# Performance work log

Measured on AMD Instinct MI355X. Metric: run time of the kernel, lower is better.

Reference implementation:

```python
import jax, jax.numpy as jnp
import numpy as np
from jax import lax

H = 1024
D = 128
T = 64  # n_step + n_middle


def gru_cell(x, h, w_ih, w_hh, b_ih, b_hh):
    # torch.nn.GRUCell gate order: r, z, n
    gi = x @ w_ih.T + b_ih
    gh = h @ w_hh.T + b_hh
    ir, iz, i_n = jnp.split(gi, 3, axis=-1)
    hr, hz, h_n = jnp.split(gh, 3, axis=-1)
    r = jax.nn.sigmoid(ir + hr)
    z = jax.nn.sigmoid(iz + hz)
    n = jnp.tanh(i_n + r * h_n)
    return (1.0 - z) * n + z * h


def decoder(z_seq, z8, n1, w_init, b_init, wi1, wh1, bi1, bh1, wi2, wh2, bi2, bh2, w_out, b_out):
    B = z_seq.shape[0]
    out0 = jnp.zeros((B, D), z_seq.dtype).at[:, -1].set(1.0)
    h0 = z8 @ w_init.T + b_init              # [B, H]
    h1 = jnp.zeros_like(h0)                  # replaced at i == 0
    xs = (jnp.arange(T), jnp.swapaxes(z_seq, 0, 1))  # ([T], [T, B, D])

    def step(carry, x):
        h0, h1, out = carry
        i, z_i = x
        inp = jnp.where(i <= n1 - 1, z_i, out)
        h0n = gru_cell(inp, h0, wi1, wh1, bi1, bh1)
        h1 = jnp.where(i == 0, h0n, h1)
        h1n = gru_cell(h0n, h1, wi2, wh2, bi2, bh2)
        out = h1n @ w_out.T + b_out          # [B, 128]
        return (h0n, h1n, out), out

    _, outs = lax.scan(step, (h0, h1, out0), xs)  # [T, B, 128]
    return jnp.swapaxes(outs[n1 - 1:], 0, 1)      # [B, T-n1+1, 128]


def _p(key, shape):
    return jax.random.normal(key, shape, dtype=jnp.float32) * 0.02


def setup_inputs() -> dict:
    key = jax.random.key(0)
    ks = jax.random.split(key, 32)
    B = 2048
    inp = {
        'zp': jax.random.normal(ks[0], (B, T, D), jnp.float32),
        'zr': jax.random.normal(ks[1], (B, T, D), jnp.float32),
        'zp8': jax.random.normal(ks[2], (B, D), jnp.float32),
        'zr8': jax.random.normal(ks[3], (B, D), jnp.float32),
        'n1': 16,
        'n2': 48,
    }
    # GRU cells 1..4: (w_ih [3H, in], w_hh [3H, H], b_ih [3H], b_hh [3H])
    for j, name in enumerate(['1', '2', '3', '4']):
        in_dim = D if name in ('1', '3') else H
        inp['wi' + name] = _p(ks[4 + 4 * j], (3 * H, in_dim))
        inp['wh' + name] = _p(ks[5 + 4 * j], (3 * H, H))
        inp['bi' + name] = _p(ks[6 + 4 * j], (3 * H,))
        inp['bh' + name] = _p(ks[7 + 4 * j], (3 * H,))
    inp['w_init0'] = _p(ks[20], (H, D)); inp['b_init0'] = _p(ks[21], (H,))
    inp['w_init1'] = _p(ks[22], (H, D)); inp['b_init1'] = _p(ks[23], (H,))
    inp['w_out0'] = _p(ks[24], (D, H)); inp['b_out0'] = _p(ks[25], (D,))
    inp['w_out1'] = _p(ks[26], (D, H)); inp['b_out1'] = _p(ks[27], (D,))
    return inp


def reference(zp, zr, zp8, zr8, n1, n2,
              wi1, wh1, bi1, bh1, wi2, wh2, bi2, bh2,
              wi3, wh3, bi3, bh3, wi4, wh4, bi4, bh4,
              w_init0, b_init0, w_init1, b_init1,
              w_out0, b_out0, w_out1, b_out1):
    z_r = decoder(zr, zr8, n1, w_init0, b_init0, wi1, wh1, bi1, bh1,
                  wi2, wh2, bi2, bh2, w_out0, b_out0)
    z_p = decoder(zp, zp8, n1, w_init1, b_init1, wi3, wh3, bi3, bh3,
                  wi4, wh4, bi4, bh4, w_out1, b_out1)
    return (z_p, z_r)
```

## Files before the change

kernel.cpp:

```cpp
#include <hip/hip_runtime.h>

typedef unsigned short u16;
typedef unsigned int u32;
typedef __attribute__((ext_vector_type(8))) short short8;
typedef __attribute__((ext_vector_type(4))) float f32x4;

#define DEV __device__ __forceinline__
#define SB0() __builtin_amdgcn_sched_barrier(0)

DEV u16 f2bf(float f){
  u32 u = __builtin_bit_cast(u32, f);
  u += 0x7fffu + ((u >> 16) & 1u);
  return (u16)(u >> 16);
}
DEV float sigm(float x){ return 1.f / (1.f + __expf(-x)); }
DEV float tanh_(float x){ return 2.f / (1.f + __expf(-2.f * x)) - 1.f; }

DEV void gl_lds16(const void* g, void* l){
  __builtin_amdgcn_global_load_lds(
      (const __attribute__((address_space(1))) u32*)g,
      (__attribute__((address_space(3))) u32*)l, 16, 0, 0);
}

#define MFMA16(A,B,C) __builtin_amdgcn_mfma_f32_16x16x32_bf16(A, B, C, 0, 0, 0)

__global__ void pack_w_kernel(const float* __restrict__ wi, const float* __restrict__ wh,
                              u16* __restrict__ dst, int Ki, int Kh, int nrows){
  const int KT = Ki + Kh;
  const long n = (long)nrows * KT;
  for (long idx = (long)blockIdx.x * blockDim.x + threadIdx.x; idx < n;
       idx += (long)gridDim.x * blockDim.x){
    int r = (int)(idx / KT), c = (int)(idx % KT);
    float v = (c < Ki) ? wi[(long)r * Ki + c] : wh[(long)r * Kh + (c - Ki)];
    dst[idx] = f2bf(v);
  }
}

struct InitA { const float* z8; const float* wini; const float* bini; float* h0f; u16* h0bf; };

__global__ __launch_bounds__(256)
void init_kernel(InitA A0, InitA A1){
  const InitA& a = (blockIdx.z == 0) ? A0 : A1;
  __shared__ float lz[64][128];
  const int tid = threadIdx.x;
  const int rb = blockIdx.x * 64, ub = blockIdx.y * 128;
  {
    const int row = tid >> 2, q = tid & 3;
    const float4* p = (const float4*)(a.z8 + (long)(rb + row) * 128 + q * 32);
    float4* dst = (float4*)&lz[row][q * 32];
    #pragma unroll
    for (int j = 0; j < 8; ++j) dst[j] = p[j];
  }
  __syncthreads();
  const int u = ub + (tid & 127);
  const int rg = tid >> 7;
  float acc[32];
  #pragma unroll
  for (int r = 0; r < 32; ++r) acc[r] = 0.f;
  for (int k = 0; k < 128; k += 4){
    float4 w4 = *(const float4*)&a.wini[(long)u * 128 + k];
    #pragma unroll
    for (int r = 0; r < 32; ++r){
      float4 z4 = *(const float4*)&lz[rg * 32 + r][k];
      acc[r] += w4.x * z4.x + w4.y * z4.y + w4.z * z4.z + w4.w * z4.w;
    }
  }
  const float b = a.bini[u];
  #pragma unroll
  for (int r = 0; r < 32; ++r){
    const long row = rb + rg * 32 + r;
    const float v = acc[r] + b;
    a.h0f[row * 1024 + u] = v;
    a.h0bf[row * 1024 + u] = f2bf(v);
  }
}

struct CellA {
  const u16* W;
  const float* bi; const float* bh;
  const float* afz; const float* afo;
  const u16* ab1; const u16* ab2;
  const float* holdr; float* holdw; u16* hbfw;
};

template<int CELL>
__global__ __attribute__((amdgpu_waves_per_eu(2, 2))) __launch_bounds__(256)
void cell_kernel(CellA A0, CellA A1, const int* dn1, int step){
  constexpr int KTOT = (CELL == 1) ? 1152 : 2048;
  constexpr int KT = KTOT / 64;
  constexpr int NI_STEPS = (CELL == 1) ? 2 : 16;

  __shared__ u16 lA[2][128 * 64];
  __shared__ u16 lB[2][192 * 64];

  const CellA& a = (blockIdx.y == 0) ? A0 : A1;
  const int tid = threadIdx.x;
  const int lane = tid & 63;
  const int wv = tid >> 6;
  const int wm = wv >> 1;
  const int wn = wv & 1;
  const int bid = blockIdx.x;
  const int inner = bid >> 3;
  const int m_idx = inner & 15;
  const int n_idx = (bid & 7) * 2 + (inner >> 4);
  const int brow = m_idx * 128;
  const int u0 = n_idx * 64;

  f32x4 aR[4][2] = {}; f32x4 aZ[4][2] = {};
  f32x4 aNI[4][2] = {}; f32x4 aNH[4][2] = {};

  const int srow = tid >> 3;
  const int sxor8 = ((tid & 7) ^ (srow & 7)) * 8;

  auto stage = [&](int bf, int kt){
    const int k0 = kt * 64;
    const u16* ab; int kk;
    if constexpr (CELL == 1){ ab = a.ab1; kk = k0 - 128; }
    else { if (k0 < 1024){ ab = a.ab1; kk = k0; } else { ab = a.ab2; kk = k0 - 1024; } }
    #pragma unroll
    for (int j = 0; j < 4; ++j)
      gl_lds16(ab + (long)(brow + j * 32 + srow) * 1024 + kk + sxor8,
               &lA[bf][(j * 32 + wv * 8) * 64]);
    #pragma unroll
    for (int j = 0; j < 6; ++j){
      const int gbase = j * 32 + wv * 8;
      const int g = gbase >> 6;
      gl_lds16(a.W + (long)(g * 1024 + u0 + ((j * 32 + srow) & 63)) * KTOT + k0 + sxor8,
               &lB[bf][(j * 32 + wv * 8) * 64]);
    }
  };

  const int l15 = lane & 15;
  const int kq = lane >> 4;
  const int sx = lane & 7;

  auto read_a_ks = [&](int bf, int ks, short8 (&af)[4]){
    const int soff = (((ks * 4 + kq) ^ sx)) * 8;
    #pragma unroll
    for (int fr = 0; fr < 4; ++fr)
      af[fr] = *(const short8*)&lA[bf][(wm * 64 + fr * 16 + l15) * 64 + soff];
  };
  auto read_b_ks = [&](int bf, int g, int ks, short8 (&bg)[2]){
    const int soff = (((ks * 4 + kq) ^ sx)) * 8;
    #pragma unroll
    for (int fc = 0; fc < 2; ++fc)
      bg[fc] = *(const short8*)&lB[bf][(g * 64 + wn * 32 + fc * 16 + l15) * 64 + soff];
  };
  auto mfma8 = [&](const short8 (&af)[4], const short8 (&bg)[2], f32x4 (&A)[4][2]){
    #pragma unroll
    for (int fr = 0; fr < 4; ++fr)
      #pragma unroll
      for (int fc = 0; fc < 2; ++fc)
        A[fr][fc] = MFMA16(af[fr], bg[fc], A[fr][fc]);
  };

  int kstart;
  if constexpr (CELL == 1){
    const int n1v = *dn1;
    const float* fsrc; long fstr;
    if (step < n1v){ fsrc = a.afz; fstr = 64 * 128; }
    else           { fsrc = a.afo; fstr = 128; }
    {
      const int row = tid >> 1, half = tid & 1;
      #pragma unroll
      for (int st = 0; st < 2; ++st){
        const float* pp = fsrc + (long)(brow + row) * fstr + st * 64 + half * 32;
        #pragma unroll
        for (int q = 0; q < 4; ++q){
          float4 x = ((const float4*)pp)[2 * q];
          float4 y = ((const float4*)pp)[2 * q + 1];
          short8 o;
          o[0] = (short)f2bf(x.x); o[1] = (short)f2bf(x.y);
          o[2] = (short)f2bf(x.z); o[3] = (short)f2bf(x.w);
          o[4] = (short)f2bf(y.x); o[5] = (short)f2bf(y.y);
          o[6] = (short)f2bf(y.z); o[7] = (short)f2bf(y.w);
          const int s = half * 4 + q;
          *(short8*)&lA[st][row * 64 + ((s ^ (row & 7)) * 8)] = o;
        }
        #pragma unroll
        for (int j = 0; j < 6; ++j){
          const int gbase = j * 32 + wv * 8;
          const int g = gbase >> 6;
          gl_lds16(a.W + (long)(g * 1024 + u0 + ((j * 32 + srow) & 63)) * KTOT + st * 64 + sxor8,
                   &lB[st][(j * 32 + wv * 8) * 64]);
        }
      }
    }
    __syncthreads();
    #pragma unroll
    for (int st = 0; st < 2; ++st){
      short8 af0[4], af1[4], b0[2], b1[2];
      read_a_ks(st, 0, af0); read_a_ks(st, 1, af1);
      read_b_ks(st, 0, 0, b0); read_b_ks(st, 0, 1, b1);
      asm volatile("s_waitcnt lgkmcnt(0)" ::: "memory"); SB0();
      mfma8(af0, b0, aR); mfma8(af1, b1, aR);
      read_b_ks(st, 1, 0, b0); read_b_ks(st, 1, 1, b1);
      asm volatile("s_waitcnt lgkmcnt(0)" ::: "memory"); SB0();
      mfma8(af0, b0, aZ); mfma8(af1, b1, aZ);
      read_b_ks(st, 2, 0, b0); read_b_ks(st, 2, 1, b1);
      asm volatile("s_waitcnt lgkmcnt(0)" ::: "memory"); SB0();
      mfma8(af0, b0, aNI); mfma8(af1, b1, aNI);
    }
    __syncthreads();
    stage(0, 2); stage(1, 3);
    kstart = 2;
  } else {
    stage(0, 0); stage(1, 1);
    kstart = 0;
  }

  for (int kt = kstart; kt < KT; ++kt){
    const int b = kt & 1;
    if (kt < KT - 1) asm volatile("s_waitcnt vmcnt(10)" ::: "memory");
    else             asm volatile("s_waitcnt vmcnt(0)" ::: "memory");
    SB0();
    __builtin_amdgcn_s_barrier();
    SB0();
    short8 af0[4], af1[4], bR0[2], bR1[2], bZ0[2], bZ1[2], bN0[2], bN1[2];
    read_a_ks(b, 0, af0); read_b_ks(b, 0, 0, bR0); SB0();
    read_b_ks(b, 1, 0, bZ0); read_b_ks(b, 2, 0, bN0); SB0();
    read_a_ks(b, 1, af1); read_b_ks(b, 0, 1, bR1); SB0();
    asm volatile("s_waitcnt lgkmcnt(10)" ::: "memory"); SB0();
    __builtin_amdgcn_s_setprio(1);
    mfma8(af0, bR0, aR);
    __builtin_amdgcn_s_setprio(0); SB0();
    read_b_ks(b, 1, 1, bZ1); read_b_ks(b, 2, 1, bN1); SB0();
    asm volatile("s_waitcnt lgkmcnt(10)" ::: "memory"); SB0();
    __builtin_amdgcn_s_setprio(1);
    mfma8(af0, bZ0, aZ);
    if (kt < NI_STEPS) mfma8(af0, bN0, aNI); else mfma8(af0, bN0, aNH);
    __builtin_amdgcn_s_setprio(0); SB0();
    asm volatile("s_waitcnt lgkmcnt(4)" ::: "memory"); SB0();
    __builtin_amdgcn_s_setprio(1);
    mfma8(af1, bR1, aR);
    __builtin_amdgcn_s_setprio(0); SB0();
    asm volatile("s_waitcnt lgkmcnt(0)" ::: "memory"); SB0();
    __builtin_amdgcn_s_barrier();
    SB0();
    if (kt + 2 < KT) stage(b, kt + 2);
    __builtin_amdgcn_s_setprio(1);
    mfma8(af1, bZ1, aZ);
    if (kt < NI_STEPS) mfma8(af1, bN1, aNI); else mfma8(af1, bN1, aNH);
    __builtin_amdgcn_s_setprio(0);
  }

  const int rq = (lane >> 4) * 4;
  #pragma unroll
  for (int fc = 0; fc < 2; ++fc){
    const int u = u0 + wn * 32 + fc * 16 + l15;
    const float br = a.bi[u] + a.bh[u];
    const float bz = a.bi[1024 + u] + a.bh[1024 + u];
    const float bni = a.bi[2048 + u];
    const float bnh = a.bh[2048 + u];
    #pragma unroll
    for (int fr = 0; fr < 4; ++fr){
      #pragma unroll
      for (int rg = 0; rg < 4; ++rg){
        const long row = brow + wm * 64 + fr * 16 + rq + rg;
        const float r = sigm(aR[fr][fc][rg] + br);
        const float z = sigm(aZ[fr][fc][rg] + bz);
        const float n = tanh_(aNI[fr][fc][rg] + bni + r * (aNH[fr][fc][rg] + bnh));
        const float hp = a.holdr[row * 1024 + u];
        const float hn = (1.f - z) * n + z * hp;
        a.holdw[row * 1024 + u] = hn;
        a.hbfw[row * 1024 + u] = f2bf(hn);
      }
    }
  }
}

struct OutA { const u16* Ah; const u16* Wo; const float* bo; float* outf; };

__global__ __launch_bounds__(256, 2)
void out_kernel(OutA A0, OutA A1, const int* dn1, int step, float* __restrict__ dout, long outhalf){
  const int n1v = *dn1;
  if (step < n1v - 1) return;
  __shared__ u16 lA[2][32 * 64];
  __shared__ u16 lB[2][128 * 64];
  const OutA& a = (blockIdx.y == 0) ? A0 : A1;
  const int tid = threadIdx.x, lane = tid & 63, wv = tid >> 6;
  const int brow = blockIdx.x * 32;
  f32x4 acc[2][2] = {};
  const int srow = tid >> 3;
  const int sxor8 = ((tid & 7) ^ (srow & 7)) * 8;

  auto stage = [&](int bf, int kt){
    const int k0 = kt * 64;
    gl_lds16(a.Ah + (long)(brow + srow) * 1024 + k0 + sxor8, &lA[bf][wv * 8 * 64]);
    #pragma unroll
    for (int j = 0; j < 4; ++j)
      gl_lds16(a.Wo + (long)(j * 32 + srow) * 1024 + k0 + sxor8,
               &lB[bf][(j * 32 + wv * 8) * 64]);
  };

  stage(0, 0); stage(1, 1);
  const int l15 = lane & 15, kq = lane >> 4, sx = lane & 7;
  for (int kt = 0; kt < 16; ++kt){
    const int b = kt & 1;
    if (kt < 15) asm volatile("s_waitcnt vmcnt(5)" ::: "memory");
    else         asm volatile("s_waitcnt vmcnt(0)" ::: "memory");
    SB0();
    __builtin_amdgcn_s_barrier();
    SB0();
    short8 af[2][2], bf2[2][2];
    #pragma unroll
    for (int ks = 0; ks < 2; ++ks){
      const int soff = (((ks * 4 + kq) ^ sx)) * 8;
      af[ks][0] = *(const short8*)&lA[b][(l15) * 64 + soff];
      af[ks][1] = *(const short8*)&lA[b][(16 + l15) * 64 + soff];
      bf2[ks][0] = *(const short8*)&lB[b][(wv * 32 + l15) * 64 + soff];
      bf2[ks][1] = *(const short8*)&lB[b][(wv * 32 + 16 + l15) * 64 + soff];
    }
    asm volatile("s_waitcnt lgkmcnt(0)" ::: "memory"); SB0();
    __builtin_amdgcn_s_barrier();
    SB0();
    if (kt + 2 < 16) stage(b, kt + 2);
    __builtin_amdgcn_s_setprio(1);
    #pragma unroll
    for (int ks = 0; ks < 2; ++ks)
      #pragma unroll
      for (int fr = 0; fr < 2; ++fr)
        #pragma unroll
        for (int fc = 0; fc < 2; ++fc)
          acc[fr][fc] = MFMA16(af[ks][fr], bf2[ks][fc], acc[fr][fc]);
    __builtin_amdgcn_s_setprio(0);
  }
  const int nst = 65 - n1v;
  const int t = step - (n1v - 1);
  const int rq = (lane >> 4) * 4;
  #pragma unroll
  for (int fc = 0; fc < 2; ++fc){
    const int u = wv * 32 + fc * 16 + l15;
    const float bo = a.bo[u];
    #pragma unroll
    for (int fr = 0; fr < 2; ++fr){
      #pragma unroll
      for (int rg = 0; rg < 4; ++rg){
        const long row = brow + fr * 16 + rq + rg;
        const float v = acc[fr][fc][rg] + bo;
        a.outf[row * 128 + u] = v;
        dout[(long)blockIdx.y * outhalf + (row * nst + t) * 128 + u] = v;
      }
    }
  }
}

extern "C" void kernel_launch(void* const* d_in, const int* in_sizes, int n_in,
                              void* d_out, int out_size, void* d_ws, size_t ws_size,
                              hipStream_t stream){
  const float* zz[2]   = { (const float*)d_in[0],  (const float*)d_in[1] };
  const float* z8[2]   = { (const float*)d_in[2],  (const float*)d_in[3] };
  const int* dn1       = (const int*)d_in[4];
  const float* wi_c1[2] = { (const float*)d_in[14], (const float*)d_in[6] };
  const float* wh_c1[2] = { (const float*)d_in[15], (const float*)d_in[7] };
  const float* bi_c1[2] = { (const float*)d_in[16], (const float*)d_in[8] };
  const float* bh_c1[2] = { (const float*)d_in[17], (const float*)d_in[9] };
  const float* wi_c2[2] = { (const float*)d_in[18], (const float*)d_in[10] };
  const float* wh_c2[2] = { (const float*)d_in[19], (const float*)d_in[11] };
  const float* bi_c2[2] = { (const float*)d_in[20], (const float*)d_in[12] };
  const float* bh_c2[2] = { (const float*)d_in[21], (const float*)d_in[13] };
  const float* wini[2]  = { (const float*)d_in[24], (const float*)d_in[22] };
  const float* bini[2]  = { (const float*)d_in[25], (const float*)d_in[23] };
  const float* wout[2]  = { (const float*)d_in[28], (const float*)d_in[26] };
  const float* bout[2]  = { (const float*)d_in[29], (const float*)d_in[27] };

  char* p = (char*)d_ws;
  auto alloc = [&](size_t bytes)->char*{
    char* q = p; p += (bytes + 255) & ~(size_t)255; return q;
  };
  u16* W1c[2]; u16* W2c[2]; u16* Woc[2];
  float* h0f[2]; float* h1f[2]; float* outf[2];
  u16* h0bf[2][2]; u16* h1bf[2][2];
  for (int d = 0; d < 2; ++d){
    W1c[d] = (u16*)alloc(3072ULL * 1152 * 2);
    W2c[d] = (u16*)alloc(3072ULL * 2048 * 2);
    Woc[d] = (u16*)alloc(128ULL * 1024 * 2);
    h0f[d] = (float*)alloc(2048ULL * 1024 * 4);
    h1f[d] = (float*)alloc(2048ULL * 1024 * 4);
    outf[d] = (float*)alloc(2048ULL * 128 * 4);
    for (int b = 0; b < 2; ++b){
      h0bf[d][b] = (u16*)alloc(2048ULL * 1024 * 2);
      h1bf[d][b] = (u16*)alloc(2048ULL * 1024 * 2);
    }
  }
  if ((size_t)(p - (char*)d_ws) > ws_size) return;

  for (int d = 0; d < 2; ++d){
    pack_w_kernel<<<dim3(1024), dim3(256), 0, stream>>>(wi_c1[d], wh_c1[d], W1c[d], 128, 1024, 3072);
    pack_w_kernel<<<dim3(1024), dim3(256), 0, stream>>>(wi_c2[d], wh_c2[d], W2c[d], 1024, 1024, 3072);
    pack_w_kernel<<<dim3(64),   dim3(256), 0, stream>>>(wout[d], wout[d], Woc[d], 1024, 0, 128);
  }
  {
    InitA I0{ z8[0], wini[0], bini[0], h0f[0], h0bf[0][0] };
    InitA I1{ z8[1], wini[1], bini[1], h0f[1], h0bf[1][0] };
    init_kernel<<<dim3(32, 8, 2), dim3(256), 0, stream>>>(I0, I1);
  }

  const long outhalf = (long)out_size / 2;

  for (int i = 0; i < 64; ++i){
    const int cur = i & 1, nxt = cur ^ 1;
    CellA c1[2], c2[2];
    for (int d = 0; d < 2; ++d){
      c1[d] = CellA{ W1c[d], bi_c1[d], bh_c1[d],
                     zz[d] + (long)i * 128, outf[d],
                     h0bf[d][cur], nullptr,
                     h0f[d], h0f[d], h0bf[d][nxt] };
      c2[d] = CellA{ W2c[d], bi_c2[d], bh_c2[d],
                     nullptr, nullptr,
                     h0bf[d][nxt], (i == 0) ? h0bf[d][nxt] : h1bf[d][cur],
                     (i == 0) ? h0f[d] : h1f[d], h1f[d], h1bf[d][nxt] };
    }
    cell_kernel<1><<<dim3(256, 2), dim3(256), 0, stream>>>(c1[0], c1[1], dn1, i);
    cell_kernel<2><<<dim3(256, 2), dim3(256), 0, stream>>>(c2[0], c2[1], dn1, i);
    OutA o0{ h1bf[0][nxt], Woc[0], bout[0], outf[0] };
    OutA o1{ h1bf[1][nxt], Woc[1], bout[1], outf[1] };
    out_kernel<<<dim3(64, 2), dim3(256), 0, stream>>>(o0, o1, dn1, i, (float*)d_out, outhalf);
  }
}
```

Measured before the change: 7.152 ms.

## Enlarge GRU cell tile to 256 rows per block with one wave per EU

Doubles the M tile of the fused GRU gate GEMM from 128 to 256 rows, so each block reuses each staged weight tile across twice as many batch rows and the grid halves to 256 blocks (128 per direction). Accumulators and A fragments double per wave, so occupancy is lowered to one wave per EU. The MFMA/LDS-read interleave is reordered so the first R-gate MFMAs issue before the second k-slice reads. The cost is fewer waves to hide latency, heavier register pressure, and a grid of 256 blocks that may leave part of the GPU idle.

```diff
diff --git a/kernel.cpp b/kernel.cpp
--- a/kernel.cpp
+++ b/kernel.cpp
@@ -84,13 +84,13 @@
 };
 
 template<int CELL>
-__global__ __attribute__((amdgpu_waves_per_eu(2, 2))) __launch_bounds__(256)
+__global__ __attribute__((amdgpu_waves_per_eu(1, 1))) __launch_bounds__(256)
 void cell_kernel(CellA A0, CellA A1, const int* dn1, int step){
   constexpr int KTOT = (CELL == 1) ? 1152 : 2048;
   constexpr int KT = KTOT / 64;
   constexpr int NI_STEPS = (CELL == 1) ? 2 : 16;
 
-  __shared__ u16 lA[2][128 * 64];
+  __shared__ u16 lA[2][256 * 64];
   __shared__ u16 lB[2][192 * 64];
 
   const CellA& a = (blockIdx.y == 0) ? A0 : A1;
@@ -101,13 +101,13 @@
   const int wn = wv & 1;
   const int bid = blockIdx.x;
   const int inner = bid >> 3;
-  const int m_idx = inner & 15;
-  const int n_idx = (bid & 7) * 2 + (inner >> 4);
-  const int brow = m_idx * 128;
+  const int m_idx = inner & 7;
+  const int n_idx = (bid & 7) * 2 + (inner >> 3);
+  const int brow = m_idx * 256;
   const int u0 = n_idx * 64;
 
-  f32x4 aR[4][2] = {}; f32x4 aZ[4][2] = {};
-  f32x4 aNI[4][2] = {}; f32x4 aNH[4][2] = {};
+  f32x4 aR[8][2] = {}; f32x4 aZ[8][2] = {};
+  f32x4 aNI[8][2] = {}; f32x4 aNH[8][2] = {};
 
   const int srow = tid >> 3;
   const int sxor8 = ((tid & 7) ^ (srow & 7)) * 8;
@@ -118,14 +118,13 @@
     if constexpr (CELL == 1){ ab = a.ab1; kk = k0 - 128; }
     else { if (k0 < 1024){ ab = a.ab1; kk = k0; } else { ab = a.ab2; kk = k0 - 1024; } }
     #pragma unroll
-    for (int j = 0; j < 4; ++j)
+    for (int j = 0; j < 8; ++j)
       gl_lds16(ab + (long)(brow + j * 32 + srow) * 1024 + kk + sxor8,
                &lA[bf][(j * 32 + wv * 8) * 64]);
     #pragma unroll
     for (int j = 0; j < 6; ++j){
-      const int gbase = j * 32 + wv * 8;
-      const int g = gbase >> 6;
-      gl_lds16(a.W + (long)(g * 1024 + u0 + ((j * 32 + srow) & 63)) * KTOT + k0 + sxor8,
+      const int g = j >> 1;
+      gl_lds16(a.W + (long)(g * 1024 + u0 + (j & 1) * 32 + srow) * KTOT + k0 + sxor8,
                &lB[bf][(j * 32 + wv * 8) * 64]);
     }
   };
@@ -134,11 +133,11 @@
   const int kq = lane >> 4;
   const int sx = lane & 7;
 
-  auto read_a_ks = [&](int bf, int ks, short8 (&af)[4]){
+  auto read_a_ks = [&](int bf, int ks, short8 (&af)[8]){
     const int soff = (((ks * 4 + kq) ^ sx)) * 8;
     #pragma unroll
-    for (int fr = 0; fr < 4; ++fr)
-      af[fr] = *(const short8*)&lA[bf][(wm * 64 + fr * 16 + l15) * 64 + soff];
+    for (int fr = 0; fr < 8; ++fr)
+      af[fr] = *(const short8*)&lA[bf][(wm * 128 + fr * 16 + l15) * 64 + soff];
   };
   auto read_b_ks = [&](int bf, int g, int ks, short8 (&bg)[2]){
     const int soff = (((ks * 4 + kq) ^ sx)) * 8;
@@ -146,9 +145,9 @@
     for (int fc = 0; fc < 2; ++fc)
       bg[fc] = *(const short8*)&lB[bf][(g * 64 + wn * 32 + fc * 16 + l15) * 64 + soff];
   };
-  auto mfma8 = [&](const short8 (&af)[4], const short8 (&bg)[2], f32x4 (&A)[4][2]){
-    #pragma unroll
-    for (int fr = 0; fr < 4; ++fr)
+  auto mfma16g = [&](const short8 (&af)[8], const short8 (&bg)[2], f32x4 (&A)[8][2]){
+    #pragma unroll
+    for (int fr = 0; fr < 8; ++fr)
       #pragma unroll
       for (int fc = 0; fc < 2; ++fc)
         A[fr][fc] = MFMA16(af[fr], bg[fc], A[fr][fc]);
@@ -161,12 +160,12 @@
     if (step < n1v){ fsrc = a.afz; fstr = 64 * 128; }
     else           { fsrc = a.afo; fstr = 128; }
     {
-      const int row = tid >> 1, half = tid & 1;
+      const int row = tid;
       #pragma unroll
       for (int st = 0; st < 2; ++st){
-        const float* pp = fsrc + (long)(brow + row) * fstr + st * 64 + half * 32;
+        const float* pp = fsrc + (long)(brow + row) * fstr + st * 64;
         #pragma unroll
-        for (int q = 0; q < 4; ++q){
+        for (int q = 0; q < 8; ++q){
           float4 x = ((const float4*)pp)[2 * q];
           float4 y = ((const float4*)pp)[2 * q + 1];
           short8 o;
@@ -174,14 +173,12 @@
           o[2] = (short)f2bf(x.z); o[3] = (short)f2bf(x.w);
           o[4] = (short)f2bf(y.x); o[5] = (short)f2bf(y.y);
           o[6] = (short)f2bf(y.z); o[7] = (short)f2bf(y.w);
-          const int s = half * 4 + q;
-          *(short8*)&lA[st][row * 64 + ((s ^ (row & 7)) * 8)] = o;
+          *(short8*)&lA[st][row * 64 + ((q ^ (row & 7)) * 8)] = o;
         }
         #pragma unroll
         for (int j = 0; j < 6; ++j){
-          const int gbase = j * 32 + wv * 8;
-          const int g = gbase >> 6;
-          gl_lds16(a.W + (long)(g * 1024 + u0 + ((j * 32 + srow) & 63)) * KTOT + st * 64 + sxor8,
+          const int g = j >> 1;
+          gl_lds16(a.W + (long)(g * 1024 + u0 + (j & 1) * 32 + srow) * KTOT + st * 64 + sxor8,
                    &lB[st][(j * 32 + wv * 8) * 64]);
         }
       }
@@ -189,17 +186,17 @@
     __syncthreads();
     #pragma unroll
     for (int st = 0; st < 2; ++st){
-      short8 af0[4], af1[4], b0[2], b1[2];
+      short8 af0[8], af1[8], b0[2], b1[2];
       read_a_ks(st, 0, af0); read_a_ks(st, 1, af1);
       read_b_ks(st, 0, 0, b0); read_b_ks(st, 0, 1, b1);
       asm volatile("s_waitcnt lgkmcnt(0)" ::: "memory"); SB0();
-      mfma8(af0, b0, aR); mfma8(af1, b1, aR);
+      mfma16g(af0, b0, aR); mfma16g(af1, b1, aR);
       read_b_ks(st, 1, 0, b0); read_b_ks(st, 1, 1, b1);
       asm volatile("s_waitcnt lgkmcnt(0)" ::: "memory"); SB0();
-      mfma8(af0, b0, aZ); mfma8(af1, b1, aZ);
+      mfma16g(af0, b0, aZ); mfma16g(af1, b1, aZ);
       read_b_ks(st, 2, 0, b0); read_b_ks(st, 2, 1, b1);
       asm volatile("s_waitcnt lgkmcnt(0)" ::: "memory"); SB0();
-      mfma8(af0, b0, aNI); mfma8(af1, b1, aNI);
+      mfma16g(af0, b0, aNI); mfma16g(af1, b1, aNI);
     }
     __syncthreads();
     stage(0, 2); stage(1, 3);
@@ -211,36 +208,36 @@
 
   for (int kt = kstart; kt < KT; ++kt){
     const int b = kt & 1;
-    if (kt < KT - 1) asm volatile("s_waitcnt vmcnt(10)" ::: "memory");
+    if (kt < KT - 1) asm volatile("s_waitcnt vmcnt(14)" ::: "memory");
     else             asm volatile("s_waitcnt vmcnt(0)" ::: "memory");
     SB0();
     __builtin_amdgcn_s_barrier();
     SB0();
-    short8 af0[4], af1[4], bR0[2], bR1[2], bZ0[2], bZ1[2], bN0[2], bN1[2];
+    short8 af0[8], af1[8], bR0[2], bR1[2], bZ0[2], bZ1[2], bN0[2], bN1[2];
     read_a_ks(b, 0, af0); read_b_ks(b, 0, 0, bR0); SB0();
     read_b_ks(b, 1, 0, bZ0); read_b_ks(b, 2, 0, bN0); SB0();
+    asm volatile("s_waitcnt lgkmcnt(4)" ::: "memory"); SB0();
+    __builtin_amdgcn_s_setprio(1);
+    mfma16g(af0, bR0, aR);
+    __builtin_amdgcn_s_setprio(0); SB0();
     read_a_ks(b, 1, af1); read_b_ks(b, 0, 1, bR1); SB0();
     asm volatile("s_waitcnt lgkmcnt(10)" ::: "memory"); SB0();
     __builtin_amdgcn_s_setprio(1);
-    mfma8(af0, bR0, aR);
+    mfma16g(af0, bZ0, aZ);
+    if (kt < NI_STEPS) mfma16g(af0, bN0, aNI); else mfma16g(af0, bN0, aNH);
     __builtin_amdgcn_s_setprio(0); SB0();
     read_b_ks(b, 1, 1, bZ1); read_b_ks(b, 2, 1, bN1); SB0();
-    asm volatile("s_waitcnt lgkmcnt(10)" ::: "memory"); SB0();
-    __builtin_amdgcn_s_setprio(1);
-    mfma8(af0, bZ0, aZ);
-    if (kt < NI_STEPS) mfma8(af0, bN0, aNI); else mfma8(af0, bN0, aNH);
-    __builtin_amdgcn_s_setprio(0); SB0();
     asm volatile("s_waitcnt lgkmcnt(4)" ::: "memory"); SB0();
     __builtin_amdgcn_s_setprio(1);
-    mfma8(af1, bR1, aR);
+    mfma16g(af1, bR1, aR);
     __builtin_amdgcn_s_setprio(0); SB0();
     asm volatile("s_waitcnt lgkmcnt(0)" ::: "memory"); SB0();
     __builtin_amdgcn_s_barrier();
     SB0();
     if (kt + 2 < KT) stage(b, kt + 2);
     __builtin_amdgcn_s_setprio(1);
-    mfma8(af1, bZ1, aZ);
-    if (kt < NI_STEPS) mfma8(af1, bN1, aNI); else mfma8(af1, bN1, aNH);
+    mfma16g(af1, bZ1, aZ);
+    if (kt < NI_STEPS) mfma16g(af1, bN1, aNI); else mfma16g(af1, bN1, aNH);
     __builtin_amdgcn_s_setprio(0);
   }
 
@@ -253,10 +250,10 @@
     const float bni = a.bi[2048 + u];
     const float bnh = a.bh[2048 + u];
     #pragma unroll
-    for (int fr = 0; fr < 4; ++fr){
+    for (int fr = 0; fr < 8; ++fr){
       #pragma unroll
       for (int rg = 0; rg < 4; ++rg){
-        const long row = brow + wm * 64 + fr * 16 + rq + rg;
+        const long row = brow + wm * 128 + fr * 16 + rq + rg;
         const float r = sigm(aR[fr][fc][rg] + br);
         const float z = sigm(aZ[fr][fc][rg] + bz);
         const float n = tanh_(aNI[fr][fc][rg] + bni + r * (aNH[fr][fc][rg] + bnh));
@@ -411,8 +408,8 @@
                      h0bf[d][nxt], (i == 0) ? h0bf[d][nxt] : h1bf[d][cur],
                      (i == 0) ? h0f[d] : h1f[d], h1f[d], h1bf[d][nxt] };
     }
-    cell_kernel<1><<<dim3(256, 2), dim3(256), 0, stream>>>(c1[0], c1[1], dn1, i);
-    cell_kernel<2><<<dim3(256, 2), dim3(256), 0, stream>>>(c2[0], c2[1], dn1, i);
+    cell_kernel<1><<<dim3(128, 2), dim3(256), 0, stream>>>(c1[0], c1[1], dn1, i);
+    cell_kernel<2><<<dim3(128, 2), dim3(256), 0, stream>>>(c2[0], c2[1], dn1, i);
     OutA o0{ h1bf[0][nxt], Woc[0], bout[0], outf[0] };
     OutA o1{ h1bf[1][nxt], Woc[1], bout[1], outf[1] };
     out_kernel<<<dim3(64, 2), dim3(256), 0, stream>>>(o0, o1, dn1, i, (float*)d_out, outhalf);
```

After: 9.645 ms. 34.8% more time.
